# Kernel tuning notes

Hardware: AMD Instinct MI355X
Metric: run time of the kernel (lower is better)

## Reference

```python
import jax, jax.numpy as jnp
import numpy as np

K_NEIGHBORS = 9
BN_EPS = 1e-5


def _bn(x, g, b, m, v):
    # inference-mode BatchNorm over channel (last) axis
    return (x - m) * (g / jnp.sqrt(v + BN_EPS)) + b


def _sincos_1d(dim, pos):
    half = dim // 2
    omega = 1.0 / (10000.0 ** (jnp.arange(half, dtype=jnp.float32) / half))
    ang = pos[:, None] * omega[None, :]
    return jnp.concatenate([jnp.sin(ang), jnp.cos(ang)], axis=1)


def _pos_embed_2d(dim, H, W):
    # standard 2D sin-cos positional embedding, (N, dim)
    yy, xx = jnp.meshgrid(jnp.arange(H, dtype=jnp.float32), jnp.arange(W, dtype=jnp.float32), indexing='ij')
    emb_h = _sincos_1d(dim // 2, yy.reshape(-1))
    emb_w = _sincos_1d(dim // 2, xx.reshape(-1))
    return jnp.concatenate([emb_h, emb_w], axis=1)


def setup_inputs() -> dict:
    key = jax.random.key(0)
    ks = jax.random.split(key, 8)
    B, C, H, W = 8, 192, 56, 56
    C2 = 2 * C
    Cg = C2 // 4  # per-group channels for grouped 1x1 conv
    x = jax.random.normal(ks[0], (B, C, H, W), jnp.float32)
    inp = {
        'x': x,
        'fc1_w': jax.random.normal(ks[1], (C, C), jnp.float32) * 0.05,
        'fc1_b': jnp.zeros((C,), jnp.float32),
        'bn1_g': jnp.ones((C,), jnp.float32),
        'bn1_b': jnp.zeros((C,), jnp.float32),
        'bn1_m': jax.random.normal(ks[2], (C,), jnp.float32) * 0.1,
        'bn1_v': jax.random.uniform(ks[3], (C,), jnp.float32, 0.5, 1.5),
        'gc_w': jax.random.normal(ks[4], (4, Cg, Cg), jnp.float32) * 0.05,  # groups=4, (g, out_pg, in_pg)
        'gc_b': jnp.zeros((C2,), jnp.float32),
        'bng_g': jnp.ones((C2,), jnp.float32),
        'bng_b': jnp.zeros((C2,), jnp.float32),
        'bng_m': jax.random.normal(ks[5], (C2,), jnp.float32) * 0.1,
        'bng_v': jax.random.uniform(ks[6], (C2,), jnp.float32, 0.5, 1.5),
        'fc2_w': jax.random.normal(ks[7], (C, C2), jnp.float32) * 0.05,
        'fc2_b': jnp.zeros((C,), jnp.float32),
        'bn2_g': jnp.ones((C,), jnp.float32),
        'bn2_b': jnp.zeros((C,), jnp.float32),
        'bn2_m': jnp.zeros((C,), jnp.float32),
        'bn2_v': jnp.ones((C,), jnp.float32),
    }
    return inp


def reference(x, fc1_w, fc1_b, bn1_g, bn1_b, bn1_m, bn1_v,
              gc_w, gc_b, bng_g, bng_b, bng_m, bng_v,
              fc2_w, fc2_b, bn2_g, bn2_b, bn2_m, bn2_v):
    B, C, H, W = x.shape
    N = H * W
    shortcut = x
    # fc1: 1x1 conv + BN, working in (B, N, C) layout
    h = x.reshape(B, C, N).transpose(0, 2, 1)
    h = jnp.einsum('bnc,dc->bnd', h, fc1_w) + fc1_b
    h = _bn(h, bn1_g, bn1_b, bn1_m, bn1_v)
    # relative position bias (ViG-style: -2*pe@pe.T/dim)
    pe = _pos_embed_2d(C, H, W)                      # (N, C)
    rel = (-2.0 / C) * (pe @ pe.T)                   # (N, N)
    # dense dilated kNN graph on L2-normalized features
    xn = h / jnp.maximum(jnp.linalg.norm(h, axis=-1, keepdims=True), 1e-12)
    sq = jnp.sum(xn * xn, axis=-1, keepdims=True)    # (B, N, 1)
    dist = sq - 2.0 * jnp.einsum('bnc,bmc->bnm', xn, xn) + sq.transpose(0, 2, 1)
    dist = dist + rel[None]                          # (B, N, N)
    _, nn_idx = jax.lax.top_k(-dist, K_NEIGHBORS)    # (B, N, K), dilation=1
    # MRConv2d: max-relative aggregation
    x_j = h[jnp.arange(B)[:, None, None], nn_idx]    # (B, N, K, C) gather
    d = jnp.max(x_j - h[:, :, None, :], axis=2)      # (B, N, C)
    g = jnp.concatenate([h, d], axis=-1)             # (B, N, 2C)
    # grouped 1x1 conv (groups=4) + BN + GELU
    C2 = 2 * C
    Cg = C2 // 4
    gg = g.reshape(B, N, 4, Cg)
    y = jnp.einsum('bngc,gdc->bngd', gg, gc_w).reshape(B, N, C2) + gc_b
    y = jax.nn.gelu(_bn(y, bng_g, bng_b, bng_m, bng_v), approximate=False)
    # fc2: 1x1 conv + BN, residual
    o = jnp.einsum('bnc,dc->bnd', y, fc2_w) + fc2_b
    o = _bn(o, bn2_g, bn2_b, bn2_m, bn2_v)
    out = o.transpose(0, 2, 1).reshape(B, C, H, W) + shortcut
    return out
```

## Files before the change

kernel.cpp:

```cpp
#include <hip/hip_runtime.h>
#include <math.h>

#define BATCH 8
#define CH    192
#define WW    56
#define NPTS  3136
#define C2    384
#define CG    96
#define MT    16
#define MSPLIT 4
#define LK    12
#define NCAND (MSPLIT*LK)
#define NREF  16
#define MQ    (NPTS/MSPLIT)

typedef float f32x4 __attribute__((ext_vector_type(4)));
typedef short bf16x8 __attribute__((ext_vector_type(8)));

__device__ __forceinline__ float gelu_exact(float v) {
  return 0.5f * v * (1.0f + erff(v * 0.7071067811865475f));
}
__device__ __forceinline__ unsigned short f2bf(float f) {
  unsigned int u = __float_as_uint(f);
  u = u + 0x7fffu + ((u >> 16) & 1u);
  return (unsigned short)(u >> 16);
}
__device__ __forceinline__ float bf2f(unsigned short h) {
  return __uint_as_float(((unsigned int)h) << 16);
}
__device__ __forceinline__ void gl_lds16(const void* g, void* lds) {
  __builtin_amdgcn_global_load_lds(
      (const __attribute__((address_space(1))) unsigned int*)g,
      (__attribute__((address_space(3))) unsigned int*)lds, 16, 0, 0);
}
__device__ __forceinline__ unsigned fmono(float f) {
  unsigned u = __float_as_uint(f);
  return u ^ ((unsigned)((int)u >> 31) | 0x80000000u);
}

__global__ void prep_kernel(
    const float* __restrict__ fc1_w, const float* __restrict__ fc1_b,
    const float* __restrict__ bn1_g, const float* __restrict__ bn1_b,
    const float* __restrict__ bn1_m, const float* __restrict__ bn1_v,
    const float* __restrict__ gc_w,  const float* __restrict__ gc_b,
    const float* __restrict__ bng_g, const float* __restrict__ bng_b,
    const float* __restrict__ bng_m, const float* __restrict__ bng_v,
    const float* __restrict__ fc2_w, const float* __restrict__ fc2_b,
    const float* __restrict__ bn2_g, const float* __restrict__ bn2_b,
    const float* __restrict__ bn2_m, const float* __restrict__ bn2_v,
    float* __restrict__ w1, float* __restrict__ b1,
    unsigned short* __restrict__ wgh, unsigned short* __restrict__ wgl,
    float* __restrict__ bg,
    unsigned short* __restrict__ w2h, unsigned short* __restrict__ w2l,
    float* __restrict__ b2, float* __restrict__ ftab)
{
  int i = blockIdx.x * 256 + threadIdx.x;
  if (i < 36864) {
    int d = i / CH;
    float s = bn1_g[d] / sqrtf(bn1_v[d] + 1e-5f);
    w1[i] = fc1_w[i] * s;
  } else if (i < 37056) {
    int d = i - 36864;
    float s = bn1_g[d] / sqrtf(bn1_v[d] + 1e-5f);
    b1[d] = (fc1_b[d] - bn1_m[d]) * s + bn1_b[d];
  } else if (i < 73920) {
    int j = i - 37056;
    int o = j / CG;
    float s = bng_g[o] / sqrtf(bng_v[o] + 1e-5f);
    float v = gc_w[j] * s;
    unsigned short hi = f2bf(v);
    wgh[j] = hi;
    wgl[j] = f2bf(v - bf2f(hi));
  } else if (i < 74304) {
    int o = i - 73920;
    float s = bng_g[o] / sqrtf(bng_v[o] + 1e-5f);
    bg[o] = (gc_b[o] - bng_m[o]) * s + bng_b[o];
  } else if (i < 148032) {
    int j = i - 74304;
    int d = j / C2;
    float s = bn2_g[d] / sqrtf(bn2_v[d] + 1e-5f);
    float v = fc2_w[j] * s;
    unsigned short hi = f2bf(v);
    w2h[j] = hi;
    w2l[j] = f2bf(v - bf2f(hi));
  } else if (i < 148224) {
    int d = i - 148032;
    float s = bn2_g[d] / sqrtf(bn2_v[d] + 1e-5f);
    b2[d] = (fc2_b[d] - bn2_m[d]) * s + bn2_b[d];
  } else if (i < 148280) {
    int delta = i - 148224;
    float s = 0.f;
    for (int t = 0; t < 48; ++t) {
      float omega = powf(10000.f, -(float)t / 48.f);
      s += cosf((float)delta * omega);
    }
    ftab[delta] = s * (-2.0f / (float)CH);
  }
}

__global__ __launch_bounds__(256) void fc1_kernel(
    const float* __restrict__ x, const float* __restrict__ w1,
    const float* __restrict__ b1, float* __restrict__ h)
{
  __shared__ float As[64*68];
  __shared__ float Bs[64*68];
  const int tid = threadIdx.x;
  const int ntile = blockIdx.x, dt = blockIdx.y, b = blockIdx.z;
  const int n0 = ntile * 64, d0 = dt * 64;
  const int ty = tid >> 4, tx = tid & 15;
  const float* xb = x + (size_t)b * CH * NPTS;
  float acc[4][4] = {};
  for (int k0 = 0; k0 < CH; k0 += 64) {
    if (k0) __syncthreads();
#pragma unroll
    for (int p = 0; p < 16; ++p) {
      int e = p * 256 + tid;
      int kk = e >> 6, r = e & 63;
      As[r*68 + kk] = xb[(size_t)(k0 + kk) * NPTS + n0 + r];
    }
#pragma unroll
    for (int p = 0; p < 4; ++p) {
      int e = p * 256 + tid;
      int dd = e >> 4, k4 = (e & 15) << 2;
      *(float4*)&Bs[dd*68 + k4] = *(const float4*)&w1[(size_t)(d0 + dd) * CH + k0 + k4];
    }
    __syncthreads();
#pragma unroll
    for (int kq = 0; kq < 16; ++kq) {
      float4 av[4], bv[4];
#pragma unroll
      for (int i = 0; i < 4; ++i) av[i] = *(const float4*)&As[(ty*4+i)*68 + kq*4];
#pragma unroll
      for (int j = 0; j < 4; ++j) bv[j] = *(const float4*)&Bs[(tx*4+j)*68 + kq*4];
#pragma unroll
      for (int i = 0; i < 4; ++i)
#pragma unroll
        for (int j = 0; j < 4; ++j)
          acc[i][j] += av[i].x*bv[j].x + av[i].y*bv[j].y + av[i].z*bv[j].z + av[i].w*bv[j].w;
    }
  }
#pragma unroll
  for (int i = 0; i < 4; ++i) {
    int n = n0 + ty*4 + i;
    float4 v;
    v.x = acc[i][0] + b1[d0 + tx*4 + 0];
    v.y = acc[i][1] + b1[d0 + tx*4 + 1];
    v.z = acc[i][2] + b1[d0 + tx*4 + 2];
    v.w = acc[i][3] + b1[d0 + tx*4 + 3];
    *(float4*)&h[((size_t)b * NPTS + n) * CH + d0 + tx*4] = v;
  }
}

__global__ __launch_bounds__(256) void norm_kernel(
    const float* __restrict__ h, float* __restrict__ xnf,
    unsigned short* __restrict__ xhi, unsigned short* __restrict__ xlo,
    float* __restrict__ sqv)
{
  const int lane = threadIdx.x & 63;
  const int row = blockIdx.x * 4 + (threadIdx.x >> 6);
  const float* hr = h + (size_t)row * CH;
  float v0 = hr[lane], v1 = hr[lane + 64], v2 = hr[lane + 128];
  float s = v0*v0 + v1*v1 + v2*v2;
#pragma unroll
  for (int o = 32; o > 0; o >>= 1) s += __shfl_xor(s, o);
  float inv = 1.0f / fmaxf(sqrtf(s), 1e-12f);
  float x0 = v0 * inv, x1 = v1 * inv, x2 = v2 * inv;
  size_t base = (size_t)row * CH;
  xnf[base + lane      ] = x0;
  xnf[base + lane + 64 ] = x1;
  xnf[base + lane + 128] = x2;
  unsigned short h0 = f2bf(x0), h1 = f2bf(x1), h2 = f2bf(x2);
  xhi[base + lane      ] = h0;
  xhi[base + lane + 64 ] = h1;
  xhi[base + lane + 128] = h2;
  xlo[base + lane      ] = f2bf(x0 - bf2f(h0));
  xlo[base + lane + 64 ] = f2bf(x1 - bf2f(h1));
  xlo[base + lane + 128] = f2bf(x2 - bf2f(h2));
  if (lane == 0) sqv[row] = s * inv * inv;
}

__global__ __launch_bounds__(256, 4) void topk_kernel(
    const unsigned short* __restrict__ xhi, const unsigned short* __restrict__ xlo,
    const float* __restrict__ fts_g,
    unsigned* __restrict__ pd)
{
  __shared__ __align__(16) char LDSbuf[2 * 12288];
  __shared__ float ft[64];

  const int tid  = threadIdx.x;
  const int lane = tid & 63;
  const int w    = tid >> 6;
  const int bid  = blockIdx.x;
  const int b    = bid & 7;
  const int r_   = bid >> 3;
  const int ms   = r_ / 49;
  const int nt   = r_ % 49;
  const int n0 = nt * 64;
  const size_t rowbase = (size_t)b * NPTS;

  if (tid < 64) ft[tid] = (tid < 56) ? fts_g[tid] : 0.0f;

  const int ar = lane & 15;
  const int hi = lane >> 4;
  const int ak = hi * 8;

  const int n_b = n0 + w * 16 + ar;
  bf16x8 bhi[6], blo[6];
  {
    const unsigned short* pbh = xhi + (rowbase + n_b) * CH + ak;
    const unsigned short* pbl = xlo + (rowbase + n_b) * CH + ak;
#pragma unroll
    for (int c = 0; c < 6; ++c) {
      bhi[c] = *(const bf16x8*)(pbh + c * 32);
      blo[c] = *(const bf16x8*)(pbl + c * 32);
    }
  }
  const int yn_l = n_b / WW, xn_l = n_b % WW;

  unsigned ld[LK];
#pragma unroll
  for (int k = 0; k < LK; ++k) ld[k] = 0xFFFFFFFFu;

  int srcb[3];
#pragma unroll
  for (int j = 0; j < 3; ++j) {
    int L = (w & 1) * 3072 + j * 1024 + lane * 16;
    int r = L / 384, off = L % 384;
    srcb[j] = r * 384 + (off ^ ((r & 7) << 4));
  }
  const int ldsb = (w >= 2 ? 6144 : 0) + (w & 1) * 3072;

  const int mbase = ms * MQ;
  const char* gb = (w < 2 ? (const char*)xhi : (const char*)xlo)
                   + (rowbase + mbase) * (CH * 2);

#define STAGE(BUF) do {                                                     \
  _Pragma("unroll")                                                         \
  for (int j = 0; j < 3; ++j)                                               \
    gl_lds16(gb + srcb[j], LDSbuf + (BUF) * 12288 + ldsb + j * 1024);       \
} while (0)

  STAGE(0);
  gb += 6144;

  int ym0 = ms * 14, xm0 = 0;

  for (int tt = 0; tt < 49; ++tt) {
    __syncthreads();
    if (tt + 1 < 49) { STAGE((tt + 1) & 1); gb += 6144; }

    const int bufb = (tt & 1) * 12288;
    const int swz = (ar & 7) << 4;
    f32x4 a_hh = {}, a_hl = {}, a_lh = {};
#pragma unroll
    for (int c = 0; c < 6; ++c) {
      int off = bufb + ar * 384 + ((c * 64 + hi * 16) ^ swz);
      bf16x8 ah = *(const bf16x8*)(LDSbuf + off);
      bf16x8 al = *(const bf16x8*)(LDSbuf + off + 6144);
      a_hh = __builtin_amdgcn_mfma_f32_16x16x32_bf16(ah, bhi[c], a_hh, 0, 0, 0);
      a_hl = __builtin_amdgcn_mfma_f32_16x16x32_bf16(ah, blo[c], a_hl, 0, 0, 0);
      a_lh = __builtin_amdgcn_mfma_f32_16x16x32_bf16(al, bhi[c], a_lh, 0, 0, 0);
    }
    f32x4 s4;
#pragma unroll
    for (int i = 0; i < 4; ++i) s4[i] = a_hh[i] + (a_hl[i] + a_lh[i]);

    const float fdy0 = ft[abs(yn_l - ym0)];
    const float fdy1 = ft[abs(yn_l - ym0 - 1)];
    const int locb = tt * MT + hi * 4;
#pragma unroll
    for (int i = 0; i < 4; ++i) {
      int xm = xm0 + hi * 4 + i;
      const bool wrap = (xm >= WW);
      if (wrap) xm -= WW;
      int dx = xn_l - xm; dx = dx < 0 ? -dx : dx;
      float d_ = (wrap ? fdy1 : fdy0) + ft[dx] - 2.0f * s4[i];
      unsigned key = (fmono(d_) & 0xFFFFFC00u) | (unsigned)(locb + i);
      if (key < ld[LK-1]) {
        unsigned cd = key;
#pragma unroll
        for (int s = 0; s < LK; ++s) {
          unsigned mn = ld[s] < cd ? ld[s] : cd;
          unsigned mx = ld[s] < cd ? cd : ld[s];
          ld[s] = mn; cd = mx;
        }
      }
    }
    xm0 += MT;
    if (xm0 >= WW) { xm0 -= WW; ym0 += 1; }
  }

  __syncthreads();
  unsigned* Md = (unsigned*)LDSbuf;
#pragma unroll
  for (int k = 0; k < LK; ++k) Md[tid * LK + k] = ld[k];
  __syncthreads();
  if (tid < 64) {
    const int wv = tid >> 4, arr = tid & 15;
    const int n = n0 + tid;
    int lb[4];
#pragma unroll
    for (int hq = 0; hq < 4; ++hq) lb[hq] = (wv * 64 + hq * 16 + arr) * LK;
    int p0 = 0, p1 = 0, p2 = 0, p3 = 0;
    unsigned* od = pd + ((rowbase + n) * MSPLIT + ms) * LK;
    for (int k = 0; k < LK; ++k) {
      unsigned bk = Md[lb[0] + p0]; int bq = 0;
      unsigned v1 = Md[lb[1] + p1];
      if (v1 < bk) { bk = v1; bq = 1; }
      unsigned v2 = Md[lb[2] + p2];
      if (v2 < bk) { bk = v2; bq = 2; }
      unsigned v3 = Md[lb[3] + p3];
      if (v3 < bk) { bk = v3; bq = 3; }
      if (bq == 0) { if (p0 < LK-1) ++p0; else Md[lb[0]+p0] = 0xFFFFFFFFu; }
      else if (bq == 1) { if (p1 < LK-1) ++p1; else Md[lb[1]+p1] = 0xFFFFFFFFu; }
      else if (bq == 2) { if (p2 < LK-1) ++p2; else Md[lb[2]+p2] = 0xFFFFFFFFu; }
      else              { if (p3 < LK-1) ++p3; else Md[lb[3]+p3] = 0xFFFFFFFFu; }
      od[k] = bk;
    }
  }
#undef STAGE
}

__global__ __launch_bounds__(256) void refine_kernel(
    const unsigned* __restrict__ pd,
    const float* __restrict__ xn, const float* __restrict__ sqv,
    const float* __restrict__ fts_g, int* __restrict__ nn)
{
  __shared__ unsigned allk[4][NCAND];
  __shared__ int      ci_s[4][NREF];
  __shared__ float ft[56];
  const int tid = threadIdx.x;
  const int w = tid >> 6, lane = tid & 63;
  if (tid < 56) ft[tid] = fts_g[tid];
  const int row = blockIdx.x * 4 + w;
  const int b = row / NPTS;
  const int n_loc = row - b * NPTS;

  if (lane < NCAND) allk[w][lane] = pd[(size_t)row * NCAND + lane];
  __syncthreads();
  if (lane < NCAND) {
    unsigned k0 = allk[w][lane];
    int rank = 0;
    for (int j = 0; j < NCAND; ++j) {
      unsigned kj = allk[w][j];
      rank += (kj < k0 || (kj == k0 && j < lane)) ? 1 : 0;
    }
    if (rank < NREF) ci_s[w][rank] = (lane / LK) * MQ + (int)(k0 & 1023u);
  }
  __syncthreads();

  const float* xrow = xn + (size_t)row * CH;
  float a0 = xrow[lane], a1 = xrow[lane + 64], a2 = xrow[lane + 128];
  const int yn_ = n_loc / WW, xq_ = n_loc % WW;
  const size_t xbase = (size_t)b * NPTS * CH;
  float myd = INFINITY; int myi = 0x7fffffff;
#pragma unroll 4
  for (int c = 0; c < NREF; ++c) {
    int m = ci_s[w][c];
    const float* xm = xn + xbase + (size_t)m * CH;
    float s = a0 * xm[lane] + a1 * xm[lane + 64] + a2 * xm[lane + 128];
#pragma unroll
    for (int o = 32; o > 0; o >>= 1) s += __shfl_xor(s, o);
    if (lane == c) {
      int ym = m / WW, xm_ = m % WW;
      int dy = yn_ - ym; dy = dy < 0 ? -dy : dy;
      int dx = xq_ - xm_; dx = dx < 0 ? -dx : dx;
      myd = sqv[(size_t)b * NPTS + m] - 2.0f * s + (ft[dy] + ft[dx]);
      myi = m;
    }
  }
  if (lane < NREF) {
    int rank = 0;
    for (int j = 0; j < NREF; ++j) {
      float dj = __shfl(myd, j); int ij = __shfl(myi, j);
      rank += (dj < myd || (dj == myd && ij < myi)) ? 1 : 0;
    }
    if (rank < 9) nn[(size_t)row * 9 + rank] = myi;
  }
}

__global__ __launch_bounds__(256) void edge_kernel(
    const float* __restrict__ h, const int* __restrict__ nn,
    float* __restrict__ df)
{
  __shared__ int nns[576];
  const int n0g = blockIdx.x * 64;
  const int b = n0g / NPTS;
  const size_t rowbase = (size_t)b * NPTS;
  const int tid = threadIdx.x;
  for (int e = tid; e < 576; e += 256)
    nns[e] = nn[(size_t)(n0g + e / 9) * 9 + (e % 9)];
  __syncthreads();
#pragma unroll
  for (int p = 0; p < 12; ++p) {
    int e = tid + 256 * p;
    int r = e / 48, c4 = (e % 48) * 4;
    float4 hv = *(const float4*)&h[(size_t)(n0g + r) * CH + c4];
    float4 mx = make_float4(-INFINITY, -INFINITY, -INFINITY, -INFINITY);
#pragma unroll
    for (int k = 0; k < 9; ++k) {
      float4 nv = *(const float4*)&h[(rowbase + nns[r*9 + k]) * CH + c4];
      mx.x = fmaxf(mx.x, nv.x); mx.y = fmaxf(mx.y, nv.y);
      mx.z = fmaxf(mx.z, nv.z); mx.w = fmaxf(mx.w, nv.w);
    }
    float4 ov;
    ov.x = mx.x - hv.x; ov.y = mx.y - hv.y; ov.z = mx.z - hv.z; ov.w = mx.w - hv.w;
    *(float4*)&df[(size_t)(n0g + r) * CH + c4] = ov;
  }
}

__global__ __launch_bounds__(256, 4) void gc_kernel(
    const float* __restrict__ h, const float* __restrict__ df,
    const unsigned short* __restrict__ wgh, const unsigned short* __restrict__ wgl,
    const float* __restrict__ bg, unsigned short* __restrict__ y)
{
  __shared__ __align__(16) char Wb[2 * 18432];
  const int tid = threadIdx.x;
  const int lane = tid & 63;
  const int w = tid >> 6;
  const int rt = blockIdx.x, g = blockIdx.y;
  const int n0g = rt * 64;
  const float* src = (g < 2) ? h : df;
  const int cb = (g & 1) * CG;
  const int cn = lane & 15;
  const int kq = lane >> 4;

  {
    const char* gh = (const char*)wgh + (size_t)g * 96 * 192;
    const char* gl = (const char*)wgl + (size_t)g * 96 * 192;
    for (int c = tid; c < 1152; c += 256) {
      int L = c * 16;
      int row = L / 192;
      int slot = (L % 192) >> 4;
      int sb = row * 192 + ((slot ^ (row & 3)) << 4);
      gl_lds16(gh + sb, Wb + L);
      gl_lds16(gl + sb, Wb + 18432 + L);
    }
  }

  const int nb = n0g + w * 16 + cn;
  const float* gr = src + (size_t)nb * CH + cb;
  bf16x8 gh8[3], gl8[3];
#pragma unroll
  for (int c = 0; c < 3; ++c) {
    float v[8];
    *(float4*)&v[0] = *(const float4*)&gr[c * 32 + kq * 8];
    *(float4*)&v[4] = *(const float4*)&gr[c * 32 + kq * 8 + 4];
#pragma unroll
    for (int j = 0; j < 8; ++j) {
      unsigned short hh = f2bf(v[j]);
      gh8[c][j] = (short)hh;
      gl8[c][j] = (short)f2bf(v[j] - bf2f(hh));
    }
  }

  __syncthreads();

#pragma unroll
  for (int sub = 0; sub < 6; ++sub) {
    f32x4 acc = {};
#pragma unroll
    for (int c = 0; c < 3; ++c) {
      int row = sub * 16 + cn;
      int slot = c * 4 + kq;
      int off = row * 192 + ((slot ^ (row & 3)) << 4);
      bf16x8 ah = *(const bf16x8*)(Wb + off);
      bf16x8 al = *(const bf16x8*)(Wb + 18432 + off);
      acc = __builtin_amdgcn_mfma_f32_16x16x32_bf16(ah, gh8[c], acc, 0, 0, 0);
      acc = __builtin_amdgcn_mfma_f32_16x16x32_bf16(ah, gl8[c], acc, 0, 0, 0);
      acc = __builtin_amdgcn_mfma_f32_16x16x32_bf16(al, gh8[c], acc, 0, 0, 0);
    }
    const int ocb = g * CG + sub * 16 + kq * 4;
    unsigned short pk[4];
#pragma unroll
    for (int i = 0; i < 4; ++i)
      pk[i] = f2bf(gelu_exact(acc[i] + bg[ocb + i]));
    *(ushort4*)&y[(size_t)nb * C2 + ocb] = *(ushort4*)pk;
  }
}

__global__ __launch_bounds__(256, 4) void fc2_kernel(
    const unsigned short* __restrict__ yv,
    const unsigned short* __restrict__ w2h, const unsigned short* __restrict__ w2l,
    const float* __restrict__ b2, const float* __restrict__ x, float* __restrict__ out)
{
  __shared__ __align__(16) char Wb[2 * 12288];
  const int tid = threadIdx.x;
  const int lane = tid & 63;
  const int w = tid >> 6;
  const int rt = blockIdx.x, dg = blockIdx.y;
  const int n0g = rt * 64;
  const int b = n0g / NPTS;
  const int nloc0 = n0g - b * NPTS;
  const int cn = lane & 15;
  const int kk0 = (lane >> 4) * 8;

  bf16x8 yb[12];
  {
    const unsigned short* yp = yv + (size_t)(n0g + w * 16 + cn) * C2 + kk0;
#pragma unroll
    for (int c = 0; c < 12; ++c) yb[c] = *(const bf16x8*)(yp + c * 32);
  }

  int srcb[3], dstb[3];
#pragma unroll
  for (int j = 0; j < 3; ++j) {
    int L = (w * 3 + j) * 1024 + lane * 16;
    int r = L / 768, off = L % 768;
    srcb[j] = r * 768 + (off ^ ((r & 7) << 4));
    dstb[j] = (w * 3 + j) * 1024;
  }

  const char* gh = (const char*)w2h + (size_t)dg * 64 * 768;
  const char* gl = (const char*)w2l + (size_t)dg * 64 * 768;
  const int rr = cn;
  const int swz = (rr & 7) << 4;
  const int nsp = nloc0 + w * 16 + cn;

  for (int ds = 0; ds < 4; ++ds) {
    __syncthreads();
#pragma unroll
    for (int j = 0; j < 3; ++j) {
      gl_lds16(gh + ds * 12288 + srcb[j], Wb + dstb[j]);
      gl_lds16(gl + ds * 12288 + srcb[j], Wb + 12288 + dstb[j]);
    }
    __syncthreads();

    f32x4 acc_h = {}, acc_l = {};
#pragma unroll
    for (int c = 0; c < 12; ++c) {
      int off = rr * 768 + ((c * 64 + (lane >> 4) * 16) ^ swz);
      bf16x8 ah = *(const bf16x8*)(Wb + off);
      bf16x8 al = *(const bf16x8*)(Wb + 12288 + off);
      acc_h = __builtin_amdgcn_mfma_f32_16x16x32_bf16(ah, yb[c], acc_h, 0, 0, 0);
      acc_l = __builtin_amdgcn_mfma_f32_16x16x32_bf16(al, yb[c], acc_l, 0, 0, 0);
    }
    const int d0 = dg * 64 + ds * 16;
#pragma unroll
    for (int i = 0; i < 4; ++i) {
      int d = d0 + (lane >> 4) * 4 + i;
      size_t gi = ((size_t)b * CH + d) * NPTS + nsp;
      out[gi] = acc_h[i] + acc_l[i] + b2[d] + x[gi];
    }
  }
}

extern "C" void kernel_launch(void* const* d_in, const int* in_sizes, int n_in,
                              void* d_out, int out_size, void* d_ws, size_t ws_size,
                              hipStream_t stream) {
  const float* x     = (const float*)d_in[0];
  const float* fc1_w = (const float*)d_in[1];
  const float* fc1_b = (const float*)d_in[2];
  const float* bn1_g = (const float*)d_in[3];
  const float* bn1_b = (const float*)d_in[4];
  const float* bn1_m = (const float*)d_in[5];
  const float* bn1_v = (const float*)d_in[6];
  const float* gc_w  = (const float*)d_in[7];
  const float* gc_b  = (const float*)d_in[8];
  const float* bng_g = (const float*)d_in[9];
  const float* bng_b = (const float*)d_in[10];
  const float* bng_m = (const float*)d_in[11];
  const float* bng_v = (const float*)d_in[12];
  const float* fc2_w = (const float*)d_in[13];
  const float* fc2_b = (const float*)d_in[14];
  const float* bn2_g = (const float*)d_in[15];
  const float* bn2_b = (const float*)d_in[16];
  const float* bn2_m = (const float*)d_in[17];
  const float* bn2_v = (const float*)d_in[18];

  float* ws = (float*)d_ws;
  size_t o = 0;
  float* W1 = ws + o; o += 36864;
  float* B1 = ws + o; o += 192;
  unsigned short* WGH = (unsigned short*)(ws + o); o += 18432;
  unsigned short* WGL = (unsigned short*)(ws + o); o += 18432;
  float* BG = ws + o; o += 384;
  unsigned short* W2H = (unsigned short*)(ws + o); o += 36864;
  unsigned short* W2L = (unsigned short*)(ws + o); o += 36864;
  float* B2 = ws + o; o += 192;
  float* FT = ws + o; o += 64;
  float* H  = ws + o; o += (size_t)25088 * 192;
  float* SQ = ws + o; o += 25088;
  int*   NN = (int*)(ws + o); o += 25088 * 9;
  float* SCR = ws + o;
  unsigned short* XHI = (unsigned short*)SCR;
  unsigned short* XLO = XHI + (size_t)4816896;
  float* DF  = SCR;
  float* XN  = SCR + (size_t)4816896;
  unsigned short* YB = (unsigned short*)XN;
  unsigned* PD = (unsigned*)(XN + (size_t)4816896);
  (void)ws_size; (void)in_sizes; (void)n_in; (void)out_size;

  hipLaunchKernelGGL(prep_kernel, dim3(580), dim3(256), 0, stream,
                     fc1_w, fc1_b, bn1_g, bn1_b, bn1_m, bn1_v,
                     gc_w, gc_b, bng_g, bng_b, bng_m, bng_v,
                     fc2_w, fc2_b, bn2_g, bn2_b, bn2_m, bn2_v,
                     W1, B1, WGH, WGL, BG, W2H, W2L, B2, FT);
  hipLaunchKernelGGL(fc1_kernel, dim3(49, 3, 8), dim3(256), 0, stream, x, W1, B1, H);
  hipLaunchKernelGGL(norm_kernel, dim3(6272), dim3(256), 0, stream, H, XN, XHI, XLO, SQ);
  hipLaunchKernelGGL(topk_kernel, dim3(49 * MSPLIT * 8), dim3(256), 0, stream, XHI, XLO, FT, PD);
  hipLaunchKernelGGL(refine_kernel, dim3(6272), dim3(256), 0, stream, PD, XN, SQ, FT, NN);
  hipLaunchKernelGGL(edge_kernel, dim3(392), dim3(256), 0, stream, H, NN, DF);
  hipLaunchKernelGGL(gc_kernel, dim3(392, 4), dim3(256), 0, stream, H, DF, WGH, WGL, BG, YB);
  hipLaunchKernelGGL(fc2_kernel, dim3(392, 3), dim3(256), 0, stream, YB, W2H, W2L, B2, x, (float*)d_out);
}
```

Before: 399.3 us.

## Fuse edge max-relative gather into grouped conv; batch top-k insertion via sorting network

Removes the separate edge_kernel and its DF buffer. The grouped-conv kernel now gathers the 9 neighbors and computes max-minus-self on the fly for groups 2 and 3, which saves a full write and re-read of the difference tensor. The top-k inner loop also changes: instead of doing up to four sequential insertion passes into the 12-entry list, it sorts the four new keys and merges them with a branch-free bitonic-style network. The merge always runs, so the early-out branch is lost and register pressure may rise.

```diff
diff --git a/kernel.cpp b/kernel.cpp
--- a/kernel.cpp
+++ b/kernel.cpp
@@ -37,6 +37,8 @@
   unsigned u = __float_as_uint(f);
   return u ^ ((unsigned)((int)u >> 31) | 0x80000000u);
 }
+__device__ __forceinline__ unsigned umin32(unsigned a, unsigned b) { return a < b ? a : b; }
+__device__ __forceinline__ unsigned umax32(unsigned a, unsigned b) { return a < b ? b : a; }
 
 __global__ void prep_kernel(
     const float* __restrict__ fc1_w, const float* __restrict__ fc1_b,
@@ -268,6 +270,7 @@
     const float fdy0 = ft[abs(yn_l - ym0)];
     const float fdy1 = ft[abs(yn_l - ym0 - 1)];
     const int locb = tt * MT + hi * 4;
+    unsigned kk[4];
 #pragma unroll
     for (int i = 0; i < 4; ++i) {
       int xm = xm0 + hi * 4 + i;
@@ -275,16 +278,38 @@
       if (wrap) xm -= WW;
       int dx = xn_l - xm; dx = dx < 0 ? -dx : dx;
       float d_ = (wrap ? fdy1 : fdy0) + ft[dx] - 2.0f * s4[i];
-      unsigned key = (fmono(d_) & 0xFFFFFC00u) | (unsigned)(locb + i);
-      if (key < ld[LK-1]) {
-        unsigned cd = key;
-#pragma unroll
-        for (int s = 0; s < LK; ++s) {
-          unsigned mn = ld[s] < cd ? ld[s] : cd;
-          unsigned mx = ld[s] < cd ? cd : ld[s];
-          ld[s] = mn; cd = mx;
-        }
-      }
+      kk[i] = (fmono(d_) & 0xFFFFFC00u) | (unsigned)(locb + i);
+    }
+    {
+      unsigned sa = umax32(kk[0], kk[1]), sb = umin32(kk[0], kk[1]);
+      unsigned sc = umax32(kk[2], kk[3]), sd = umin32(kk[2], kk[3]);
+      unsigned v0 = umax32(sa, sc), t1 = umin32(sa, sc);
+      unsigned t2 = umax32(sb, sd), v3 = umin32(sb, sd);
+      unsigned v1 = umax32(t1, t2), v2 = umin32(t1, t2);
+      unsigned l4 = umin32(ld[4], v0), g4 = umax32(ld[4], v0);
+      unsigned l5 = umin32(ld[5], v1), g5 = umax32(ld[5], v1);
+      unsigned l6 = umin32(ld[6], v2), g6 = umax32(ld[6], v2);
+      unsigned l7 = umin32(ld[7], v3), g7 = umax32(ld[7], v3);
+      unsigned a0 = umin32(ld[0], l4), b0 = umax32(ld[0], l4);
+      unsigned a1 = umin32(ld[1], l5), b1 = umax32(ld[1], l5);
+      unsigned a2 = umin32(ld[2], l6), b2 = umax32(ld[2], l6);
+      unsigned a3 = umin32(ld[3], l7), b3 = umax32(ld[3], l7);
+      unsigned q0 = umin32(a0, a2), q2 = umax32(a0, a2);
+      unsigned q1 = umin32(a1, a3), q3 = umax32(a1, a3);
+      unsigned r0 = umin32(b0, b2), r2 = umax32(b0, b2);
+      unsigned r1 = umin32(b1, b3), r3 = umax32(b1, b3);
+      ld[0] = umin32(q0, q1); ld[1] = umax32(q0, q1);
+      ld[2] = umin32(q2, q3); ld[3] = umax32(q2, q3);
+      ld[4] = umin32(r0, r1); ld[5] = umax32(r0, r1);
+      ld[6] = umin32(r2, r3); ld[7] = umax32(r2, r3);
+      unsigned e0 = umin32(ld[8],  g4);
+      unsigned e1 = umin32(ld[9],  g5);
+      unsigned e2 = umin32(ld[10], g6);
+      unsigned e3 = umin32(ld[11], g7);
+      unsigned f0 = umin32(e0, e2), f2 = umax32(e0, e2);
+      unsigned f1 = umin32(e1, e3), f3 = umax32(e1, e3);
+      ld[8]  = umin32(f0, f1); ld[9]  = umax32(f0, f1);
+      ld[10] = umin32(f2, f3); ld[11] = umax32(f2, f3);
     }
     xm0 += MT;
     if (xm0 >= WW) { xm0 -= WW; ym0 += 1; }
@@ -379,51 +404,24 @@
   }
 }
 
-__global__ __launch_bounds__(256) void edge_kernel(
+__global__ __launch_bounds__(256, 4) void gc_kernel(
     const float* __restrict__ h, const int* __restrict__ nn,
-    float* __restrict__ df)
-{
-  __shared__ int nns[576];
-  const int n0g = blockIdx.x * 64;
-  const int b = n0g / NPTS;
-  const size_t rowbase = (size_t)b * NPTS;
-  const int tid = threadIdx.x;
-  for (int e = tid; e < 576; e += 256)
-    nns[e] = nn[(size_t)(n0g + e / 9) * 9 + (e % 9)];
-  __syncthreads();
-#pragma unroll
-  for (int p = 0; p < 12; ++p) {
-    int e = tid + 256 * p;
-    int r = e / 48, c4 = (e % 48) * 4;
-    float4 hv = *(const float4*)&h[(size_t)(n0g + r) * CH + c4];
-    float4 mx = make_float4(-INFINITY, -INFINITY, -INFINITY, -INFINITY);
-#pragma unroll
-    for (int k = 0; k < 9; ++k) {
-      float4 nv = *(const float4*)&h[(rowbase + nns[r*9 + k]) * CH + c4];
-      mx.x = fmaxf(mx.x, nv.x); mx.y = fmaxf(mx.y, nv.y);
-      mx.z = fmaxf(mx.z, nv.z); mx.w = fmaxf(mx.w, nv.w);
-    }
-    float4 ov;
-    ov.x = mx.x - hv.x; ov.y = mx.y - hv.y; ov.z = mx.z - hv.z; ov.w = mx.w - hv.w;
-    *(float4*)&df[(size_t)(n0g + r) * CH + c4] = ov;
-  }
-}
-
-__global__ __launch_bounds__(256, 4) void gc_kernel(
-    const float* __restrict__ h, const float* __restrict__ df,
     const unsigned short* __restrict__ wgh, const unsigned short* __restrict__ wgl,
     const float* __restrict__ bg, unsigned short* __restrict__ y)
 {
   __shared__ __align__(16) char Wb[2 * 18432];
+  __shared__ int nns[576];
   const int tid = threadIdx.x;
   const int lane = tid & 63;
   const int w = tid >> 6;
   const int rt = blockIdx.x, g = blockIdx.y;
   const int n0g = rt * 64;
-  const float* src = (g < 2) ? h : df;
+  const int b = n0g / NPTS;
+  const size_t rowbase = (size_t)b * NPTS;
   const int cb = (g & 1) * CG;
   const int cn = lane & 15;
   const int kq = lane >> 4;
+  const bool isD = (g >= 2);
 
   {
     const char* gh = (const char*)wgh + (size_t)g * 96 * 192;
@@ -437,15 +435,39 @@
       gl_lds16(gl + sb, Wb + 18432 + L);
     }
   }
-
-  const int nb = n0g + w * 16 + cn;
-  const float* gr = src + (size_t)nb * CH + cb;
+  if (isD) {
+    for (int e = tid; e < 576; e += 256)
+      nns[e] = nn[(size_t)(n0g + e / 9) * 9 + (e % 9)];
+  }
+  __syncthreads();
+
+  const int rloc = w * 16 + cn;
+  const int nb = n0g + rloc;
   bf16x8 gh8[3], gl8[3];
 #pragma unroll
   for (int c = 0; c < 3; ++c) {
+    const float* base = h + (size_t)nb * CH + cb + c * 32 + kq * 8;
+    float4 x0 = *(const float4*)base;
+    float4 x1 = *(const float4*)(base + 4);
+    if (isD) {
+      float4 m0 = make_float4(-INFINITY, -INFINITY, -INFINITY, -INFINITY);
+      float4 m1 = m0;
+#pragma unroll
+      for (int k = 0; k < 9; ++k) {
+        const float* nbase = h + (rowbase + nns[rloc * 9 + k]) * CH + cb + c * 32 + kq * 8;
+        float4 n0v = *(const float4*)nbase;
+        float4 n1v = *(const float4*)(nbase + 4);
+        m0.x = fmaxf(m0.x, n0v.x); m0.y = fmaxf(m0.y, n0v.y);
+        m0.z = fmaxf(m0.z, n0v.z); m0.w = fmaxf(m0.w, n0v.w);
+        m1.x = fmaxf(m1.x, n1v.x); m1.y = fmaxf(m1.y, n1v.y);
+        m1.z = fmaxf(m1.z, n1v.z); m1.w = fmaxf(m1.w, n1v.w);
+      }
+      x0.x = m0.x - x0.x; x0.y = m0.y - x0.y; x0.z = m0.z - x0.z; x0.w = m0.w - x0.w;
+      x1.x = m1.x - x1.x; x1.y = m1.y - x1.y; x1.z = m1.z - x1.z; x1.w = m1.w - x1.w;
+    }
     float v[8];
-    *(float4*)&v[0] = *(const float4*)&gr[c * 32 + kq * 8];
-    *(float4*)&v[4] = *(const float4*)&gr[c * 32 + kq * 8 + 4];
+    *(float4*)&v[0] = x0;
+    *(float4*)&v[4] = x1;
 #pragma unroll
     for (int j = 0; j < 8; ++j) {
       unsigned short hh = f2bf(v[j]);
@@ -453,8 +475,6 @@
       gl8[c][j] = (short)f2bf(v[j] - bf2f(hh));
     }
   }
-
-  __syncthreads();
 
 #pragma unroll
   for (int sub = 0; sub < 6; ++sub) {
@@ -585,7 +605,6 @@
   float* SCR = ws + o;
   unsigned short* XHI = (unsigned short*)SCR;
   unsigned short* XLO = XHI + (size_t)4816896;
-  float* DF  = SCR;
   float* XN  = SCR + (size_t)4816896;
   unsigned short* YB = (unsigned short*)XN;
   unsigned* PD = (unsigned*)(XN + (size_t)4816896);
@@ -600,7 +619,6 @@
   hipLaunchKernelGGL(norm_kernel, dim3(6272), dim3(256), 0, stream, H, XN, XHI, XLO, SQ);
   hipLaunchKernelGGL(topk_kernel, dim3(49 * MSPLIT * 8), dim3(256), 0, stream, XHI, XLO, FT, PD);
   hipLaunchKernelGGL(refine_kernel, dim3(6272), dim3(256), 0, stream, PD, XN, SQ, FT, NN);
-  hipLaunchKernelGGL(edge_kernel, dim3(392), dim3(256), 0, stream, H, NN, DF);
-  hipLaunchKernelGGL(gc_kernel, dim3(392, 4), dim3(256), 0, stream, H, DF, WGH, WGL, BG, YB);
+  hipLaunchKernelGGL(gc_kernel, dim3(392, 4), dim3(256), 0, stream, H, NN, WGH, WGL, BG, YB);
   hipLaunchKernelGGL(fc2_kernel, dim3(392, 3), dim3(256), 0, stream, YB, W2H, W2L, B2, x, (float*)d_out);
 }
```

After: 369.4 us. -7.5%, faster.
